# Optimization experiments

Hardware: AMD Instinct MI355X
Metric: run time of the kernel (lower is better)

## Reference

```python
import jax, jax.numpy as jnp
import numpy as np

B, T, D = 16, 512, 384
DUR_MAX = 8            # durations in [0, DUR_MAX)
MAX_OUT = T * (DUR_MAX - 1)  # static upper bound on expanded length (3584)


def setup_inputs() -> dict:
    key = jax.random.key(0)
    kx, kd = jax.random.split(key)
    x = jax.random.normal(kx, (B, T, D), dtype=jnp.float32)
    dur = jax.random.randint(kd, (B, T), 0, DUR_MAX, dtype=jnp.int32)
    return {"x": x, "dur": dur}


def reference(x, dur):
    # Torch semantics: for each batch item, repeat frame i of x `round(dur[i])`
    # times, concatenate, then zero-pad all items to the batch max length.
    # Vectorized: cumsum of durations gives segment ends; output slot j maps to
    # source frame = searchsorted(ends, j, 'right'); slots >= total are padding.
    ends = jnp.cumsum(dur, axis=1)                      # [B, T]
    totals = ends[:, -1]                                # [B]
    j = jnp.arange(MAX_OUT, dtype=dur.dtype)            # [MAX_OUT]
    # per-batch searchsorted: src[b, j] = index of frame covering output slot j
    src = jax.vmap(lambda e: jnp.searchsorted(e, j, side='right'))(ends)
    src = jnp.minimum(src, T - 1)                       # clamp padding region
    valid = (j[None, :] < totals[:, None])              # [B, MAX_OUT]
    out = jnp.take_along_axis(x, src[:, :, None], axis=1)  # [B, MAX_OUT, D]
    return out * valid[:, :, None].astype(x.dtype)
```

## Files before the change

### kernel.cpp

```cpp
#include <hip/hip_runtime.h>


#define B_       16
#define T_       512
#define D_       384
#define MAX_OUT_ 3584
#define ROW_F4   (D_ / 4)
#define ROWS_PB  64
#define BLK_PB   (MAX_OUT_ / ROWS_PB)
#define F4_PB    (ROWS_PB * ROW_F4)

__global__ __launch_bounds__(256) void lr_fused_kernel(
    const float4* __restrict__ x4, const int* __restrict__ dur,
    float4* __restrict__ out4) {
  const int b  = blockIdx.y;
  const int r0 = blockIdx.x * ROWS_PB;
  const int t  = threadIdx.x;

  __shared__ int ends[T_];
  __shared__ int srcs[ROWS_PB];
  __shared__ int wsum[4];

  const int2 dd = ((const int2*)dur)[b * (T_ / 2) + t];
  int s = dd.x + dd.y;
  const int lane = t & 63;
  const int wave = t >> 6;
  int v = s;
  #pragma unroll
  for (int off = 1; off < 64; off <<= 1) {
    int n = __shfl_up(v, off, 64);
    if (lane >= off) v += n;
  }
  if (lane == 63) wsum[wave] = v;
  __syncthreads();
  int wpre = 0;
  #pragma unroll
  for (int w = 0; w < 3; ++w)
    if (w < wave) wpre += wsum[w];
  const int e1 = v + wpre;
  ends[2 * t]     = e1 - dd.y;
  ends[2 * t + 1] = e1;
  __syncthreads();

  if (t < ROWS_PB) {
    const int j = r0 + t;
    int lo = 0;
    #pragma unroll
    for (int step = 256; step > 0; step >>= 1)
      if (lo + step <= T_ && ends[lo + step - 1] <= j) lo += step;
    srcs[t] = (j < ends[T_ - 1]) ? lo : -1;
  }
  __syncthreads();

  const float4* __restrict__ xb = x4 + (size_t)b * T_ * ROW_F4;
  float4* __restrict__ ob = out4 + ((size_t)b * MAX_OUT_ + r0) * ROW_F4;
  #pragma unroll
  for (int k = 0; k < F4_PB / 256; ++k) {
    const int idx = k * 256 + t;
    const int rl  = idx / ROW_F4;
    const int col = idx - rl * ROW_F4;
    const int src = srcs[rl];
    float4 val = make_float4(0.f, 0.f, 0.f, 0.f);
    if (src >= 0) val = xb[src * ROW_F4 + col];
    ob[idx] = val;
  }
}

extern "C" void kernel_launch(void* const* d_in, const int* in_sizes, int n_in,
                              void* d_out, int out_size, void* d_ws, size_t ws_size,
                              hipStream_t stream) {
  const float* x   = (const float*)d_in[0];
  const int*   dur = (const int*)d_in[1];
  float* out = (float*)d_out;

  dim3 grid(BLK_PB, B_);
  lr_fused_kernel<<<grid, 256, 0, stream>>>(
      (const float4*)x, dur, (float4*)out);
}
```

Before: 20.68 us.

## Scatter source indices directly from segment bounds and halve rows per block

Instead of writing the cumsum to shared memory and binary-searching it per output row, each thread scatters its two frame indices into the block's row window using its own segment start and end. One barrier and the search are removed. Rows per block drop from 64 to 32, doubling the grid and the redundant per-block prefix scan. The gather becomes branchless: it always loads a clamped row and multiplies by a mask, so padding rows now read x (row 0) instead of skipping the load. Multiplying by the mask turns NaN or Inf values in x into NaN in padding rows rather than zero.

```diff
diff --git a/kernel.cpp b/kernel.cpp
--- a/kernel.cpp
+++ b/kernel.cpp
@@ -6,7 +6,7 @@
 #define D_       384
 #define MAX_OUT_ 3584
 #define ROW_F4   (D_ / 4)
-#define ROWS_PB  64
+#define ROWS_PB  32
 #define BLK_PB   (MAX_OUT_ / ROWS_PB)
 #define F4_PB    (ROWS_PB * ROW_F4)
 
@@ -17,38 +17,36 @@
   const int r0 = blockIdx.x * ROWS_PB;
   const int t  = threadIdx.x;
 
-  __shared__ int ends[T_];
   __shared__ int srcs[ROWS_PB];
   __shared__ int wsum[4];
 
   const int2 dd = ((const int2*)dur)[b * (T_ / 2) + t];
-  int s = dd.x + dd.y;
   const int lane = t & 63;
   const int wave = t >> 6;
-  int v = s;
+  int v = dd.x + dd.y;
   #pragma unroll
   for (int off = 1; off < 64; off <<= 1) {
     int n = __shfl_up(v, off, 64);
     if (lane >= off) v += n;
   }
   if (lane == 63) wsum[wave] = v;
+  if (t < ROWS_PB) srcs[t] = -1;
   __syncthreads();
   int wpre = 0;
   #pragma unroll
   for (int w = 0; w < 3; ++w)
     if (w < wave) wpre += wsum[w];
-  const int e1 = v + wpre;
-  ends[2 * t]     = e1 - dd.y;
-  ends[2 * t + 1] = e1;
-  __syncthreads();
+  const int e1   = v + wpre;
+  const int end0 = e1 - dd.y;
+  const int st0  = end0 - dd.x;
 
-  if (t < ROWS_PB) {
-    const int j = r0 + t;
-    int lo = 0;
-    #pragma unroll
-    for (int step = 256; step > 0; step >>= 1)
-      if (lo + step <= T_ && ends[lo + step - 1] <= j) lo += step;
-    srcs[t] = (j < ends[T_ - 1]) ? lo : -1;
+  {
+    const int lo0 = st0  > r0 ? st0  : r0;
+    const int hi0 = end0 < r0 + ROWS_PB ? end0 : r0 + ROWS_PB;
+    for (int k = lo0; k < hi0; ++k) srcs[k - r0] = 2 * t;
+    const int lo1 = end0 > r0 ? end0 : r0;
+    const int hi1 = e1   < r0 + ROWS_PB ? e1   : r0 + ROWS_PB;
+    for (int k = lo1; k < hi1; ++k) srcs[k - r0] = 2 * t + 1;
   }
   __syncthreads();
 
@@ -60,8 +58,10 @@
     const int rl  = idx / ROW_F4;
     const int col = idx - rl * ROW_F4;
     const int src = srcs[rl];
-    float4 val = make_float4(0.f, 0.f, 0.f, 0.f);
-    if (src >= 0) val = xb[src * ROW_F4 + col];
+    const int srow = src > 0 ? src : 0;
+    float4 val = xb[srow * ROW_F4 + col];
+    const float m = src >= 0 ? 1.0f : 0.0f;
+    val.x *= m; val.y *= m; val.z *= m; val.w *= m;
     ob[idx] = val;
   }
 }
```

After: 21.84 us. 5.6% more time.
